# Kernel optimization log

Hardware: AMD Instinct MI355X
Metric: run time of the kernel (lower is better)

The kernel has to match this reference:

```python
import jax, jax.numpy as jnp
import numpy as np

B, S, H = 2, 1024, 4544
NH, HD = 71, 64          # 71 query heads, head_dim 64, 1 shared kv head (multi-query)
THETA = 10000.0
NEG_INF = -1e9


def setup_inputs() -> dict:
    key = jax.random.key(0)
    k1, k2, k3 = jax.random.split(key, 3)
    hidden_states = jax.random.normal(k1, (B, S, H), dtype=jnp.float32)
    W_qkv = jax.random.normal(k2, (H, H + 2 * HD), dtype=jnp.float32) * 0.02
    W_dense = jax.random.normal(k3, (H, H), dtype=jnp.float32) * 0.02
    causal = jnp.tril(jnp.ones((S, S), dtype=bool))
    attention_mask = jnp.where(causal, 0.0, NEG_INF).astype(jnp.float32)[None, None]  # [1,1,S,S]
    position_ids = jnp.arange(S, dtype=jnp.int32)[None]  # [1,S]
    return {"hidden_states": hidden_states, "W_qkv": W_qkv, "W_dense": W_dense,
            "attention_mask": attention_mask, "position_ids": position_ids}


def _rope_cos_sin(position_ids):
    # HF FalconRotaryEmbedding: inv_freq over even dims, emb = cat(freqs, freqs)
    inv_freq = 1.0 / (THETA ** (jnp.arange(0, HD, 2, dtype=jnp.float32) / HD))
    freqs = position_ids.astype(jnp.float32)[..., None] * inv_freq  # [1,S,HD/2]
    emb = jnp.concatenate([freqs, freqs], axis=-1)                  # [1,S,HD]
    return jnp.cos(emb)[:, None], jnp.sin(emb)[:, None]             # [1,1,S,HD]


def _rotate_half(x):
    return jnp.concatenate([-x[..., HD // 2:], x[..., :HD // 2]], axis=-1)


def reference(hidden_states, W_qkv, W_dense, attention_mask, position_ids):
    # fused QKV projection (bias=False for Falcon-7B)
    fused = hidden_states @ W_qkv                       # [B,S,(NH+2)*HD]
    fused = fused.reshape(B, S, NH + 2, HD)
    q = jnp.transpose(fused[:, :, :NH], (0, 2, 1, 3))          # [B,NH,S,HD]
    k = jnp.transpose(fused[:, :, NH:NH + 1], (0, 2, 1, 3))    # [B,1,S,HD]
    v = jnp.transpose(fused[:, :, NH + 1:], (0, 2, 1, 3))      # [B,1,S,HD]

    cos, sin = _rope_cos_sin(position_ids)
    q = q * cos + _rotate_half(q) * sin
    k = k * cos + _rotate_half(k) * sin

    # scores: shared kv head broadcasts across the 71 query heads
    scores = jnp.matmul(q, jnp.swapaxes(k, -1, -2)) * (1.0 / np.sqrt(HD))  # [B,NH,S,S]
    probs = jax.nn.softmax(scores + attention_mask, axis=-1)
    attn = jnp.matmul(probs, v)                                            # [B,NH,S,HD]

    attn = jnp.transpose(attn, (0, 2, 1, 3)).reshape(B, S, NH * HD)
    return attn @ W_dense
```

## Files before the change

kernel.cpp:

```cpp
#include <hip/hip_runtime.h>

typedef unsigned short u16;
using f32x4  = __attribute__((ext_vector_type(4))) float;
using f32x16 = __attribute__((ext_vector_type(16))) float;
using s16x8  = __attribute__((ext_vector_type(8))) short;

static __device__ __forceinline__ u16 f2b(float f) {
  unsigned int u = __builtin_bit_cast(unsigned int, f);
  u = (u + 0x7fffu + ((u >> 16) & 1u)) >> 16;
  return (u16)u;
}
static __device__ __forceinline__ float b2f(u16 h) {
  unsigned int u = ((unsigned int)h) << 16;
  return __builtin_bit_cast(float, u);
}
static __device__ __forceinline__ unsigned int cvtpk(float lo, float hi) {
  unsigned int r;
  asm("v_cvt_pk_bf16_f32 %0, %1, %2" : "=v"(r) : "v"(lo), "v"(hi));
  return r;
}
static __device__ __forceinline__ void gload16(const void* g, void* l) {
  __builtin_amdgcn_global_load_lds(
      (const __attribute__((address_space(1))) void*)g,
      (__attribute__((address_space(3))) void*)l, 16, 0, 0);
}

__global__ __launch_bounds__(256) void conv_bf16(
    const float* __restrict__ in, u16* __restrict__ out, int n8)
{
  int i = blockIdx.x * 256 + threadIdx.x;
  if (i >= n8) return;
  float4 a = *(const float4*)(in + (size_t)i * 8);
  float4 b = *(const float4*)(in + (size_t)i * 8 + 4);
  __align__(16) u16 tmp[8] = {f2b(a.x), f2b(a.y), f2b(a.z), f2b(a.w),
                              f2b(b.x), f2b(b.y), f2b(b.z), f2b(b.w)};
  *(uint4*)(out + (size_t)i * 8) = *(const uint4*)tmp;
}

__global__ __launch_bounds__(256) void transpose_conv(
    const float* __restrict__ W, u16* __restrict__ Wt, int K, int N)
{
  __shared__ u16 tile[64][72];
  const int t = threadIdx.x;
  const int n0 = blockIdx.x * 64, k0 = blockIdx.y * 64;
  #pragma unroll
  for (int i = 0; i < 4; ++i) {
    int idx = i * 256 + t;
    int r = idx >> 4;
    int c = (idx & 15) << 2;
    float4 v = make_float4(0.f, 0.f, 0.f, 0.f);
    if (n0 + c < N) v = *(const float4*)(W + (size_t)(k0 + r) * N + n0 + c);
    tile[r][c + 0] = f2b(v.x);
    tile[r][c + 1] = f2b(v.y);
    tile[r][c + 2] = f2b(v.z);
    tile[r][c + 3] = f2b(v.w);
  }
  __syncthreads();
  #pragma unroll
  for (int i = 0; i < 2; ++i) {
    int idx = i * 256 + t;
    int rn = idx >> 3;
    int c8 = (idx & 7) << 3;
    __align__(16) u16 tmp[8];
    #pragma unroll
    for (int j = 0; j < 8; ++j) tmp[j] = tile[c8 + j][rn];
    *(uint4*)(Wt + (size_t)(n0 + rn) * K + k0 + c8) = *(const uint4*)tmp;
  }
}

template<int MODE>
__global__ __launch_bounds__(256) void gemm_bt(
    const u16* __restrict__ A, const u16* __restrict__ B,
    float* __restrict__ Cptr,
    u16* __restrict__ qo, u16* __restrict__ ko, u16* __restrict__ vo,
    const int* __restrict__ pos,
    int M, int N, int K, int NBX)
{
  __shared__ __align__(16) u16 aLds[3][128 * 32];
  __shared__ __align__(16) u16 bLds[3][128 * 32];

  const int t = threadIdx.x, lane = t & 63, w = t >> 6;
  const int lr = lane & 15, lg = lane >> 4;
  const int wr = w >> 1, wc = w & 1;

  const int bid = blockIdx.x;
  const int qq  = gridDim.x >> 3;
  const int swz = (bid & 7) * qq + (bid >> 3);
  const int m0 = (swz / NBX) * 128, n0 = (swz % NBX) * 128;

  const int srow = lane >> 2;
  const int skc  = (lane & 3) << 3;

  f32x4 acc[4][4] = {};
  const int nk = K >> 5;

#define STAGE(buf, tt) do {                                                   \
    size_t kq_ = (size_t)(tt) << 5;                                           \
    _Pragma("unroll")                                                         \
    for (int i_ = 0; i_ < 2; ++i_) {                                          \
      int row_ = i_ * 64 + w * 16 + srow;                                     \
      gload16(A + (size_t)(m0 + row_) * K + kq_ + skc,                        \
              (char*)&aLds[buf][0] + i_ * 4096 + w * 1024);                   \
      gload16(B + (size_t)(n0 + row_) * K + kq_ + skc,                        \
              (char*)&bLds[buf][0] + i_ * 4096 + w * 1024);                   \
    }                                                                         \
  } while (0)

  STAGE(0, 0);
  if (nk > 1) STAGE(1, 1);

  int cur = 0;
  for (int kt = 0; kt < nk; ++kt) {
    const int nx2 = cur >= 1 ? cur - 1 : cur + 2;
    if (kt + 2 < nk) {
      STAGE(nx2, kt + 2);
      asm volatile("s_waitcnt vmcnt(8)" ::: "memory");
    } else if (kt + 1 < nk) {
      asm volatile("s_waitcnt vmcnt(4)" ::: "memory");
    } else {
      asm volatile("s_waitcnt vmcnt(0)" ::: "memory");
    }
    __builtin_amdgcn_s_barrier();
    __builtin_amdgcn_sched_barrier(0);
    const u16* ab = &aLds[cur][0];
    const u16* bb = &bLds[cur][0];
    s16x8 af[4], bf[4];
    #pragma unroll
    for (int m = 0; m < 4; ++m)
      af[m] = *(const s16x8*)(ab + (wr * 64 + m * 16 + lr) * 32 + lg * 8);
    #pragma unroll
    for (int n = 0; n < 4; ++n)
      bf[n] = *(const s16x8*)(bb + (wc * 64 + n * 16 + lr) * 32 + lg * 8);
    #pragma unroll
    for (int m = 0; m < 4; ++m)
      #pragma unroll
      for (int n = 0; n < 4; ++n)
        acc[m][n] = __builtin_amdgcn_mfma_f32_16x16x32_bf16(af[m], bf[n], acc[m][n], 0, 0, 0);
    __builtin_amdgcn_s_barrier();
    cur = cur < 2 ? cur + 1 : 0;
  }
#undef STAGE

  if constexpr (MODE == 0) {
    #pragma unroll
    for (int m = 0; m < 4; ++m) {
      int row = m0 + wr * 64 + m * 16 + lg * 4;
      #pragma unroll
      for (int n = 0; n < 4; ++n) {
        int col = n0 + wc * 64 + n * 16 + lr;
        if (col < N) {
          #pragma unroll
          for (int r = 0; r < 4; ++r)
            Cptr[(size_t)(row + r) * N + col] = acc[m][n][r];
        }
      }
    }
  } else {
    const int h = (n0 + wc * 64) >> 6;
    if (h > 72) return;
    const float inv0 = exp2f(-0.41524101186092029f * (float)lr);
    const float inv1 = exp2f(-0.41524101186092029f * (float)(16 + lr));
    #pragma unroll
    for (int m = 0; m < 4; ++m) {
      #pragma unroll
      for (int r = 0; r < 4; ++r) {
        int row = m0 + wr * 64 + m * 16 + lg * 4 + r;
        int b = row >> 10, s = row & 1023;
        if (h == 72) {
          #pragma unroll
          for (int n = 0; n < 4; ++n) {
            int d = n * 16 + lr;
            vo[((size_t)b * 64 + d) * 1024 + s] = f2b(acc[m][n][r]);
          }
        } else {
          float p = (float)pos[s];
          float sn0, cs0, sn1, cs1;
          __sincosf(p * inv0, &sn0, &cs0);
          __sincosf(p * inv1, &sn1, &cs1);
          #pragma unroll
          for (int n = 0; n < 4; ++n) {
            float cs  = (n & 1) ? cs1 : cs0;
            float sn  = (n & 1) ? sn1 : sn0;
            float sgn = (n < 2) ? -1.f : 1.f;
            float val = acc[m][n][r] * cs + sgn * acc[m][n ^ 2][r] * sn;
            int d = n * 16 + lr;
            if (h < 71)
              qo[((size_t)(b * 71 + h) * 1024 + s) * 64 + d] = f2b(val);
            else
              ko[((size_t)b * 1024 + s) * 64 + d] = f2b(val);
          }
        }
      }
    }
  }
}

__global__ __launch_bounds__(128) void attn_kernel(
    const u16* __restrict__ q, const u16* __restrict__ kx,
    const u16* __restrict__ vT, u16* __restrict__ attnO)
{
  const int t = threadIdx.x, lane = t & 63, w = t >> 6;
  const int lq  = lane & 31;
  const int hi  = lane >> 5;
  const int hi4 = hi << 2;
  const int pair = blockIdx.x, h = blockIdx.y, b = blockIdx.z;
  const int qt = w ? (31 - pair) : pair;
  const int q0 = qt * 32;

  const u16* qbase = q + ((size_t)(b * 71 + h) * 1024 + q0 + lq) * 64 + hi * 8;
  s16x8 qf[4];
  #pragma unroll
  for (int kt = 0; kt < 4; ++kt) qf[kt] = *(const s16x8*)(qbase + kt * 16);

  f32x16 o0 = {}, o1 = {};
  float m = -1e30f, l = 0.f;

  const u16* kbase  = kx + ((size_t)b * 1024 + lq) * 64 + hi * 8;
  const u16* vbase0 = vT + ((size_t)b * 64 + lq) * 1024 + hi * 8;
  const u16* vbase1 = vbase0 + 32 * 1024;

  for (int it = 0; it <= qt; ++it) {
    const int kv0 = it * 32;
    s16x8 kf[4];
    #pragma unroll
    for (int kt = 0; kt < 4; ++kt)
      kf[kt] = *(const s16x8*)(kbase + (size_t)kv0 * 64 + kt * 16);
    s16x8 v00 = *(const s16x8*)(vbase0 + kv0);
    s16x8 v01 = *(const s16x8*)(vbase0 + kv0 + 16);
    s16x8 v10 = *(const s16x8*)(vbase1 + kv0);
    s16x8 v11 = *(const s16x8*)(vbase1 + kv0 + 16);

    f32x16 sa = {}, sb = {};
    sa = __builtin_amdgcn_mfma_f32_32x32x16_bf16(kf[0], qf[0], sa, 0, 0, 0);
    sb = __builtin_amdgcn_mfma_f32_32x32x16_bf16(kf[1], qf[1], sb, 0, 0, 0);
    sa = __builtin_amdgcn_mfma_f32_32x32x16_bf16(kf[2], qf[2], sa, 0, 0, 0);
    sb = __builtin_amdgcn_mfma_f32_32x32x16_bf16(kf[3], qf[3], sb, 0, 0, 0);

    float s[16];
    float pmax = -1e30f;
    if (it == qt) {
      #pragma unroll
      for (int r = 0; r < 16; ++r) {
        int R = (r & 3) + ((r >> 2) << 3) + hi4;
        s[r] = (R > lq) ? -1e30f : (sa[r] + sb[r]) * 0.125f;
        pmax = fmaxf(pmax, s[r]);
      }
    } else {
      #pragma unroll
      for (int r = 0; r < 16; ++r) {
        s[r] = (sa[r] + sb[r]) * 0.125f;
        pmax = fmaxf(pmax, s[r]);
      }
    }
    pmax = fmaxf(pmax, __shfl_xor(pmax, 32));

    if (!__all(pmax <= m + 8.f)) {
      float mn = fmaxf(m, pmax);
      float corr = __expf(m - mn);
      m = mn;
      l *= corr;
      #pragma unroll
      for (int r = 0; r < 16; ++r) {
        float c2 = __shfl(corr, (r & 3) + ((r >> 2) << 3) + hi4);
        o0[r] *= c2; o1[r] *= c2;
      }
    }

    float p[16], sum = 0.f;
    #pragma unroll
    for (int r = 0; r < 16; ++r) { p[r] = __expf(s[r] - m); sum += p[r]; }
    sum += __shfl_xor(sum, 32);
    l += sum;

    unsigned int a0 = cvtpk(p[0], p[1]),   a1 = cvtpk(p[2], p[3]);
    unsigned int b0 = cvtpk(p[4], p[5]),   b1 = cvtpk(p[6], p[7]);
    asm("v_permlane32_swap_b32 %0, %1" : "+v"(a0), "+v"(b0));
    asm("v_permlane32_swap_b32 %0, %1" : "+v"(a1), "+v"(b1));
    unsigned int c0 = cvtpk(p[8], p[9]),   c1 = cvtpk(p[10], p[11]);
    unsigned int d0 = cvtpk(p[12], p[13]), d1 = cvtpk(p[14], p[15]);
    asm("v_permlane32_swap_b32 %0, %1" : "+v"(c0), "+v"(d0));
    asm("v_permlane32_swap_b32 %0, %1" : "+v"(c1), "+v"(d1));
    union { unsigned int wd[4]; s16x8 v; } palo, pahi;
    palo.wd[0] = a0; palo.wd[1] = a1; palo.wd[2] = b0; palo.wd[3] = b1;
    pahi.wd[0] = c0; pahi.wd[1] = c1; pahi.wd[2] = d0; pahi.wd[3] = d1;

    o0 = __builtin_amdgcn_mfma_f32_32x32x16_bf16(palo.v, v00, o0, 0, 0, 0);
    o0 = __builtin_amdgcn_mfma_f32_32x32x16_bf16(pahi.v, v01, o0, 0, 0, 0);
    o1 = __builtin_amdgcn_mfma_f32_32x32x16_bf16(palo.v, v10, o1, 0, 0, 0);
    o1 = __builtin_amdgcn_mfma_f32_32x32x16_bf16(pahi.v, v11, o1, 0, 0, 0);
  }

  float linv = 1.f / l;
  #pragma unroll
  for (int r = 0; r < 16; ++r) {
    int R = (r & 3) + ((r >> 2) << 3) + hi4;
    float c2 = __shfl(linv, R);
    size_t base = ((size_t)(b * 1024 + q0 + R) * 71 + h) * 64;
    attnO[base + lq]      = f2b(o0[r] * c2);
    attnO[base + 32 + lq] = f2b(o1[r] * c2);
  }
}

extern "C" void kernel_launch(void* const* d_in, const int* in_sizes, int n_in,
                              void* d_out, int out_size, void* d_ws, size_t ws_size,
                              hipStream_t stream) {
  const float* hidden = (const float*)d_in[0];
  const float* Wqkv   = (const float*)d_in[1];
  const float* Wdense = (const float*)d_in[2];
  const int*   pos    = (const int*)d_in[4];
  float* out = (float*)d_out;

  char* wsp = (char*)d_ws;
  u16* Wt    = (u16*)(wsp);
  u16* A1    = (u16*)(wsp + 43040768);
  u16* qws   = (u16*)(wsp + 43040768 + 18612224);
  u16* kws   = (u16*)(wsp + 43040768 + 18612224 + 18612224);
  u16* vws   = (u16*)(wsp + 43040768 + 18612224 + 18612224 + 262144);
  u16* attnw = A1;

  conv_bf16<<<4544, 256, 0, stream>>>(hidden, A1, 2048 * 4544 / 8);
  transpose_conv<<<dim3(74, 71), 256, 0, stream>>>(Wqkv, Wt, 4544, 4672);
  gemm_bt<2><<<592, 256, 0, stream>>>(A1, Wt, nullptr, qws, kws, vws, pos,
                                      2048, 4672, 4544, 37);
  transpose_conv<<<dim3(72, 71), 256, 0, stream>>>(Wdense, Wt, 4544, 4544);
  attn_kernel<<<dim3(16, 71, 2), 128, 0, stream>>>(qws, kws, vws, attnw);
  gemm_bt<0><<<576, 256, 0, stream>>>(attnw, Wt, out, nullptr, nullptr, nullptr,
                                      nullptr, 2048, 4544, 4544, 36);
}
```

Before: 387.2 us.

## Merge prep kernels, fold dense-weight transpose into attention, swizzle GEMM LDS

```diff
diff --git a/kernel.cpp b/kernel.cpp
--- a/kernel.cpp
+++ b/kernel.cpp
@@ -10,10 +10,6 @@
   u = (u + 0x7fffu + ((u >> 16) & 1u)) >> 16;
   return (u16)u;
 }
-static __device__ __forceinline__ float b2f(u16 h) {
-  unsigned int u = ((unsigned int)h) << 16;
-  return __builtin_bit_cast(float, u);
-}
 static __device__ __forceinline__ unsigned int cvtpk(float lo, float hi) {
   unsigned int r;
   asm("v_cvt_pk_bf16_f32 %0, %1, %2" : "=v"(r) : "v"(lo), "v"(hi));
@@ -25,27 +21,14 @@
       (__attribute__((address_space(3))) void*)l, 16, 0, 0);
 }
 
-__global__ __launch_bounds__(256) void conv_bf16(
-    const float* __restrict__ in, u16* __restrict__ out, int n8)
+template<int NT>
+static __device__ __forceinline__ void transpose_tile(
+    const float* __restrict__ W, u16* __restrict__ Wt, int K, int N,
+    int n0, int k0, int t, u16 (*tile)[72])
 {
-  int i = blockIdx.x * 256 + threadIdx.x;
-  if (i >= n8) return;
-  float4 a = *(const float4*)(in + (size_t)i * 8);
-  float4 b = *(const float4*)(in + (size_t)i * 8 + 4);
-  __align__(16) u16 tmp[8] = {f2b(a.x), f2b(a.y), f2b(a.z), f2b(a.w),
-                              f2b(b.x), f2b(b.y), f2b(b.z), f2b(b.w)};
-  *(uint4*)(out + (size_t)i * 8) = *(const uint4*)tmp;
-}
-
-__global__ __launch_bounds__(256) void transpose_conv(
-    const float* __restrict__ W, u16* __restrict__ Wt, int K, int N)
-{
-  __shared__ u16 tile[64][72];
-  const int t = threadIdx.x;
-  const int n0 = blockIdx.x * 64, k0 = blockIdx.y * 64;
   #pragma unroll
-  for (int i = 0; i < 4; ++i) {
-    int idx = i * 256 + t;
+  for (int i = 0; i < 1024 / NT; ++i) {
+    int idx = i * NT + t;
     int r = idx >> 4;
     int c = (idx & 15) << 2;
     float4 v = make_float4(0.f, 0.f, 0.f, 0.f);
@@ -57,14 +40,34 @@
   }
   __syncthreads();
   #pragma unroll
-  for (int i = 0; i < 2; ++i) {
-    int idx = i * 256 + t;
+  for (int i = 0; i < 512 / NT; ++i) {
+    int idx = i * NT + t;
     int rn = idx >> 3;
     int c8 = (idx & 7) << 3;
     __align__(16) u16 tmp[8];
     #pragma unroll
     for (int j = 0; j < 8; ++j) tmp[j] = tile[c8 + j][rn];
     *(uint4*)(Wt + (size_t)(n0 + rn) * K + k0 + c8) = *(const uint4*)tmp;
+  }
+}
+
+__global__ __launch_bounds__(256) void prep_kernel(
+    const float* __restrict__ hidden, u16* __restrict__ A1,
+    const float* __restrict__ Wqkv, u16* __restrict__ Wt)
+{
+  __shared__ u16 tile[64][72];
+  const int bid = blockIdx.x, t = threadIdx.x;
+  if (bid < 4544) {
+    int i = bid * 256 + t;
+    float4 a = *(const float4*)(hidden + (size_t)i * 8);
+    float4 b = *(const float4*)(hidden + (size_t)i * 8 + 4);
+    __align__(16) u16 tmp[8] = {f2b(a.x), f2b(a.y), f2b(a.z), f2b(a.w),
+                                f2b(b.x), f2b(b.y), f2b(b.z), f2b(b.w)};
+    *(uint4*)(A1 + (size_t)i * 8) = *(const uint4*)tmp;
+  } else {
+    int tb = bid - 4544;
+    int n0 = (tb % 74) * 64, k0 = (tb / 74) * 64;
+    transpose_tile<256>(Wqkv, Wt, 4544, 4672, n0, k0, t, tile);
   }
 }
 
@@ -89,7 +92,7 @@
   const int m0 = (swz / NBX) * 128, n0 = (swz % NBX) * 128;
 
   const int srow = lane >> 2;
-  const int skc  = (lane & 3) << 3;
+  const int ssl  = ((lane & 3) ^ ((lane >> 3) & 3)) << 3;
 
   f32x4 acc[4][4] = {};
   const int nk = K >> 5;
@@ -99,9 +102,9 @@
     _Pragma("unroll")                                                         \
     for (int i_ = 0; i_ < 2; ++i_) {                                          \
       int row_ = i_ * 64 + w * 16 + srow;                                     \
-      gload16(A + (size_t)(m0 + row_) * K + kq_ + skc,                        \
+      gload16(A + (size_t)(m0 + row_) * K + kq_ + ssl,                        \
               (char*)&aLds[buf][0] + i_ * 4096 + w * 1024);                   \
-      gload16(B + (size_t)(n0 + row_) * K + kq_ + skc,                        \
+      gload16(B + (size_t)(n0 + row_) * K + kq_ + ssl,                        \
               (char*)&bLds[buf][0] + i_ * 4096 + w * 1024);                   \
     }                                                                         \
   } while (0)
@@ -109,6 +112,7 @@
   STAGE(0, 0);
   if (nk > 1) STAGE(1, 1);
 
+  const int sl = (lg ^ ((lr >> 1) & 3)) << 3;
   int cur = 0;
   for (int kt = 0; kt < nk; ++kt) {
     const int nx2 = cur >= 1 ? cur - 1 : cur + 2;
@@ -127,10 +131,10 @@
     s16x8 af[4], bf[4];
     #pragma unroll
     for (int m = 0; m < 4; ++m)
-      af[m] = *(const s16x8*)(ab + (wr * 64 + m * 16 + lr) * 32 + lg * 8);
+      af[m] = *(const s16x8*)(ab + (wr * 64 + m * 16 + lr) * 32 + sl);
     #pragma unroll
     for (int n = 0; n < 4; ++n)
-      bf[n] = *(const s16x8*)(bb + (wc * 64 + n * 16 + lr) * 32 + lg * 8);
+      bf[n] = *(const s16x8*)(bb + (wc * 64 + n * 16 + lr) * 32 + sl);
     #pragma unroll
     for (int m = 0; m < 4; ++m)
       #pragma unroll
@@ -195,15 +199,24 @@
   }
 }
 
-__global__ __launch_bounds__(128) void attn_kernel(
+__global__ __launch_bounds__(128) void attn_plus(
     const u16* __restrict__ q, const u16* __restrict__ kx,
-    const u16* __restrict__ vT, u16* __restrict__ attnO)
+    const u16* __restrict__ vT, u16* __restrict__ attnO,
+    const float* __restrict__ Wd, u16* __restrict__ Wt)
 {
+  __shared__ u16 tile[64][72];
+  const int bid = blockIdx.x;
+  if (bid >= 2272) {
+    int tb = bid - 2272;
+    int n0 = (tb % 72) * 64, k0 = (tb / 72) * 64;
+    transpose_tile<128>(Wd, Wt, 4544, 4544, n0, k0, threadIdx.x, tile);
+    return;
+  }
   const int t = threadIdx.x, lane = t & 63, w = t >> 6;
   const int lq  = lane & 31;
   const int hi  = lane >> 5;
   const int hi4 = hi << 2;
-  const int pair = blockIdx.x, h = blockIdx.y, b = blockIdx.z;
+  const int pair = bid & 15, h = (bid >> 4) % 71, b = bid / 1136;
   const int qt = w ? (31 - pair) : pair;
   const int q0 = qt * 32;
 
@@ -318,12 +331,10 @@
   u16* vws   = (u16*)(wsp + 43040768 + 18612224 + 18612224 + 262144);
   u16* attnw = A1;
 
-  conv_bf16<<<4544, 256, 0, stream>>>(hidden, A1, 2048 * 4544 / 8);
-  transpose_conv<<<dim3(74, 71), 256, 0, stream>>>(Wqkv, Wt, 4544, 4672);
+  prep_kernel<<<4544 + 5254, 256, 0, stream>>>(hidden, A1, Wqkv, Wt);
   gemm_bt<2><<<592, 256, 0, stream>>>(A1, Wt, nullptr, qws, kws, vws, pos,
                                       2048, 4672, 4544, 37);
-  transpose_conv<<<dim3(72, 71), 256, 0, stream>>>(Wdense, Wt, 4544, 4544);
-  attn_kernel<<<dim3(16, 71, 2), 128, 0, stream>>>(qws, kws, vws, attnw);
+  attn_plus<<<2272 + 5112, 128, 0, stream>>>(qws, kws, vws, attnw, Wdense, Wt);
   gemm_bt<0><<<576, 256, 0, stream>>>(attnw, Wt, out, nullptr, nullptr, nullptr,
                                       nullptr, 2048, 4544, 4544, 36);
 }
```

Measured after the change: 384.4 us. About the same (-0.7%).
